# Kernel optimization log

Hardware: AMD Instinct MI355X
Metric: run time of the kernel (lower is better)

## Reference

```python
import jax, jax.numpy as jnp
import numpy as np

NE, EW, TOP_K, T_D, MAXNNZ = 32, 2944, 4, 8, 256
ALPHA, LIMIT, ORIG = 1.702, 7.0, 2880
HID = 2048


def setup_inputs() -> dict:
    key = jax.random.key(0)
    ks = jax.random.split(key, 7)
    dt = jnp.float16
    hid = jax.random.normal(ks[0], (1, 1024, HID), dtype=dt)
    # rand_init() sets all params to torch.rand(...)/5 -> Uniform[0, 0.2)
    gate_w = (jax.random.uniform(ks[1], (NE, HID), dtype=dt) * 0.2).astype(dt)
    u = (jax.random.uniform(ks[2], (NE * EW, HID), dtype=dt) * 0.2).astype(dt)
    g = (jax.random.uniform(ks[3], (NE * EW, HID), dtype=dt) * 0.2).astype(dt)
    d = (jax.random.uniform(ks[4], (HID, NE * EW), dtype=dt) * 0.2).astype(dt)
    ub = (jax.random.uniform(ks[5], (NE * EW,), dtype=dt) * 0.2).astype(dt)
    gb = (jax.random.uniform(ks[6], (NE * EW,), dtype=dt) * 0.2).astype(dt)
    return {"hid": hid, "gate_w": gate_w, "u": u, "g": g, "d": d, "ub": ub, "gb": gb}


def _act(up, gate):
    # clamped GLU: gate clamped above, up clamped both sides; glu = g*sigmoid(alpha*g); (up+1)*glu
    gate = jnp.minimum(gate, LIMIT)
    up = jnp.clip(up, -LIMIT, LIMIT)
    glu = gate * jax.nn.sigmoid(gate * ALPHA)
    act = (up + 1.0) * glu
    return act.at[..., ORIG:].set(0)  # padded inter dims (2880..2944) zeroed


def _forward(hid, gate_w, u, g, d, ub, gb):
    B, S, H = hid.shape
    x = hid.reshape(-1, H)           # [bs, H]
    bs = x.shape[0]

    # --- routing: softmax -> top-k -> renormalize -> scatter to sparse weights ---
    logits = (x @ gate_w.T).astype(jnp.float32)          # [bs, NE]
    probs = jax.nn.softmax(logits, axis=1)
    vals, idx = jax.lax.top_k(probs, TOP_K)
    vals = vals / vals.sum(axis=1, keepdims=True)
    sparse_rw = jnp.zeros_like(probs).at[jnp.arange(bs)[:, None], idx].set(vals)
    rw = sparse_rw.astype(x.dtype)                        # [bs, NE]

    # --- expert selection: t_d dense experts + t_d sparse experts by load ---
    routing_n = jnp.count_nonzero(rw, axis=0)
    mask_c = jax.lax.top_k(routing_n, 2 * T_D)[1]         # [2*T_D]
    cd, cs = mask_c[:T_D], mask_c[T_D:]
    # top-MAXNNZ tokens per sparse expert
    mask_r = jax.lax.top_k(sparse_rw[:, cs].T, MAXNNZ)[1].T  # [MAXNNZ, T_D]

    U = u.reshape(NE, EW, H)
    G = g.reshape(NE, EW, H)
    UB = ub.reshape(NE, EW)
    GB = gb.reshape(NE, EW)
    D = d.reshape(H, NE, EW)

    # --- dense experts: every token runs through the t_d hottest experts ---
    up_d = jnp.einsum('nh,teh->nte', x, U[cd]) + UB[cd]   # [bs, T_D, EW]
    gt_d = jnp.einsum('nh,teh->nte', x, G[cd]) + GB[cd]
    act_d = _act(up_d, gt_d) * rw[:, cd][..., None]       # routing weight combine
    out = jnp.einsum('nte,hte->nh', act_d, D[:, cd])      # [bs, H]

    # --- sparse experts: gather top-MAXNNZ tokens, MLP, scatter-add back ---
    xs = x[mask_r]                                        # [M, T_D, H]
    up_s = jnp.einsum('mth,teh->mte', xs, U[cs]) + UB[cs]
    gt_s = jnp.einsum('mth,teh->mte', xs, G[cs]) + GB[cs]
    w_s = rw[mask_r, cs[None, :]]                         # [M, T_D]
    act_s = _act(up_s, gt_s) * w_s[..., None]
    contrib = jnp.einsum('mte,hte->mth', act_s, D[:, cs])  # [M, T_D, H]
    out = out.at[mask_r.reshape(-1)].add(contrib.reshape(-1, H))

    return out.reshape(B, S, H)


def reference(hid, gate_w, u, g, d, ub, gb):
    return _forward(hid, gate_w, u, g, d, ub, gb)
```

## Files before the change

### kernel.cpp

```cpp
#include <hip/hip_runtime.h>

#define HID 2048
#define NE_ 32
#define EW_ 2944
#define ORIG_ 2880
#define TOPK_ 4
#define MAXNNZ_ 256
#define BS_ 1024
#define NEWTOT (NE_*EW_)

typedef unsigned short u16;
typedef _Float16 h8  __attribute__((ext_vector_type(8)));
typedef float  f32x4 __attribute__((ext_vector_type(4)));
typedef float  fv4   __attribute__((ext_vector_type(4)));

__device__ __forceinline__ u16 f2h_bits(float f){
  union{ _Float16 h; u16 u; } c; c.h = (_Float16)f; return c.u;
}
__device__ __forceinline__ float f16q(float f){ return (float)(_Float16)f; }

__device__ __forceinline__ h8 cvt8(fv4 a, fv4 b){
  h8 r;
  r[0]=(_Float16)a[0]; r[1]=(_Float16)a[1]; r[2]=(_Float16)a[2]; r[3]=(_Float16)a[3];
  r[4]=(_Float16)b[0]; r[5]=(_Float16)b[1]; r[6]=(_Float16)b[2]; r[7]=(_Float16)b[3];
  return r;
}
__device__ __forceinline__ int ldsx(int row, int chunk){
  return row*32 + ((chunk ^ ((row>>1)&3))*8);
}

__device__ __forceinline__ void barrier_lgkm(){
  asm volatile("s_waitcnt lgkmcnt(0)" ::: "memory");
  __builtin_amdgcn_s_barrier();
  __builtin_amdgcn_sched_barrier(0);
}

__device__ __forceinline__ int rank_kth(const int* counts, int kth){
  int cnt[NE_]; bool used[NE_];
  for (int e=0;e<NE_;e++){ cnt[e]=counts[e]; used[e]=false; }
  int bi=0;
  for (int k=0;k<=kth;k++){
    int best=-1; bi=0;
    for (int e=0;e<NE_;e++) if(!used[e] && cnt[e]>best){best=cnt[e];bi=e;}
    used[bi]=true;
  }
  return bi;
}

__global__ __launch_bounds__(256) void k_gate(const float* __restrict__ x,
                                              const float* __restrict__ gw,
                                              float* __restrict__ rw,
                                              float* __restrict__ rwf,
                                              int* __restrict__ counts,
                                              u16* __restrict__ xh)
{
  __shared__ float slog[4][NE_];
  const int tid = threadIdx.x, wid = tid>>6, lane = tid&63;
  const int n = blockIdx.x*4 + wid;
  const float* xr = x + (size_t)n*HID + lane*32;
  float xf[32];
  #pragma unroll
  for (int i=0;i<8;i++){
    fv4 v = *(const fv4*)(xr + i*4);
    #pragma unroll
    for (int j=0;j<4;j++) xf[i*4+j] = v[j];
  }
  #pragma unroll
  for (int c=0;c<4;c++){
    h8 hv;
    #pragma unroll
    for (int j=0;j<8;j++) hv[j] = (_Float16)xf[c*8+j];
    *(h8*)(xh + (size_t)n*HID + lane*32 + c*8) = hv;
  }
  for (int e=0;e<NE_;e++){
    const float* gr = gw + (size_t)e*HID + lane*32;
    float p = 0.f;
    #pragma unroll
    for (int i=0;i<8;i++){
      fv4 v = *(const fv4*)(gr + i*4);
      #pragma unroll
      for (int j=0;j<4;j++) p += xf[i*4+j]*v[j];
    }
    #pragma unroll
    for (int s=32;s>0;s>>=1) p += __shfl_xor(p, s);
    if (lane==0) slog[wid][e] = f16q(p);
  }
  if (lane==0){
    float mx=-1e30f;
    for (int e=0;e<NE_;e++) mx = fmaxf(mx, slog[wid][e]);
    float pr[NE_]; float sum=0.f;
    for (int e=0;e<NE_;e++){ float v=__expf(slog[wid][e]-mx); pr[e]=v; sum+=v; }
    for (int e=0;e<NE_;e++) pr[e] = pr[e]/sum;
    int   idx[TOPK_]; float val[TOPK_]; bool used[NE_];
    for (int e=0;e<NE_;e++) used[e]=false;
    float vs=0.f;
    for (int k=0;k<TOPK_;k++){
      float best=-1.f; int bi=0;
      for (int e=0;e<NE_;e++) if(!used[e] && pr[e]>best){best=pr[e];bi=e;}
      used[bi]=true; idx[k]=bi; val[k]=best; vs+=best;
    }
    float* rwr  = rw  + (size_t)n*NE_;
    float* rwfr = rwf + (size_t)n*NE_;
    for (int k=0;k<TOPK_;k++){
      float vraw = val[k]/vs;
      float q = f16q(vraw);
      rwr[idx[k]]  = q;
      rwfr[idx[k]] = vraw;
      if (q!=0.f) atomicAdd(counts+idx[k], 1);
    }
  }
}

__global__ __launch_bounds__(256) void k_lists(const float* __restrict__ rw,
                                               const float* __restrict__ rwf,
                                               const int* __restrict__ counts,
                                               int* __restrict__ cdcs,
                                               int* __restrict__ tok_all,
                                               int* __restrict__ cnt_all,
                                               int* __restrict__ inv,
                                               int* __restrict__ invcnt)
{
  __shared__ float v[BS_];
  __shared__ int scnt;
  __shared__ int e_sh;
  const int z = blockIdx.x;
  const int tid = threadIdx.x;
  if (tid==0){
    int e = rank_kth(counts, z);
    e_sh = e;
    cdcs[z] = e;
    scnt = 0;
  }
  for (int i=tid;i<BS_;i+=256) tok_all[z*BS_+i] = 0;
  __syncthreads();
  const int e = e_sh;
  for (int i=tid;i<BS_;i+=256) v[i] = (z<8) ? rw[(size_t)i*NE_+e] : rwf[(size_t)i*NE_+e];
  __syncthreads();
  for (int i=tid;i<BS_;i+=256){
    bool take;
    if (z<8){
      take = (v[i]!=0.f);
    } else {
      float vi=v[i]; int r=0;
      for (int m=0;m<BS_;m++){
        float vm=v[m];
        r += (vm>vi) || (vm==vi && m<i);
      }
      take = (r<MAXNNZ_) && (rw[(size_t)i*NE_+e]!=0.f);
    }
    if (take){
      int slot = atomicAdd(&scnt,1);
      tok_all[z*BS_+slot] = i;
      int c = atomicAdd(&invcnt[i],1);
      inv[i*4+c] = (z<<16) | slot;
    }
  }
  __syncthreads();
  if (tid==0) cnt_all[z] = scnt;
}

__global__ __launch_bounds__(256, 4) void k_fused(const u16* __restrict__ xh,
                                               const float* __restrict__ uw,
                                               const float* __restrict__ gww,
                                               const float* __restrict__ ub,
                                               const float* __restrict__ gb,
                                               const float* __restrict__ rw,
                                               const int* __restrict__ cdcs,
                                               const int* __restrict__ tok_all,
                                               const int* __restrict__ cnt_all,
                                               u16* __restrict__ act)
{
  const int z=blockIdx.z, bx=blockIdx.x, by=blockIdx.y;
  const int cnt = cnt_all[z];
  if (by*128 >= cnt) return;
  const int e = cdcs[z];
  __shared__ __align__(16) u16 ldsA[2][128*32];
  __shared__ __align__(16) u16 ldsB[2][64*32];
  const int tid=threadIdx.x, lane=tid&63, w=tid>>6;
  const int lr = lane&15, kq = lane>>4;

  const int ar = tid>>1, c0 = (tid&1)*2;
  const int tokA = tok_all[z*BS_ + by*128 + ar];
  const u16* ap = xh + (size_t)tokA*HID + c0*8;
  const int br = tid>>2, bch = tid&3;
  const float* bp = (br<32 ? uw  + ((size_t)e*EW_ + bx*32 + br)*HID
                           : gww + ((size_t)e*EW_ + bx*32 + (br-32))*HID) + bch*8;

  f32x4 au[2][2], ag[2][2];
  #pragma unroll
  for (int i=0;i<2;i++)
    #pragma unroll
    for (int j=0;j<2;j++)
      #pragma unroll
      for (int q=0;q<4;q++){ au[i][j][q]=0.f; ag[i][j][q]=0.f; }

  h8 As0, As1; fv4 Ba, Bb;
  As0 = *(const h8*)ap; As1 = *(const h8*)(ap+8);
  Ba = *(const fv4*)bp; Bb = *(const fv4*)(bp+4);

  const int NK = HID/32;
  #pragma unroll 2
  for (int kt=0; kt<NK; kt++){
    u16* A = ldsA[kt&1]; u16* B = ldsB[kt&1];
    *(h8*)&A[ldsx(ar, c0  )] = As0;
    *(h8*)&A[ldsx(ar, c0+1)] = As1;
    *(h8*)&B[ldsx(br, bch)] = cvt8(Ba,Bb);
    if (kt+1<NK){
      const int k1=(kt+1)*32;
      As0 = *(const h8*)(ap+k1); As1 = *(const h8*)(ap+k1+8);
      Ba=*(const fv4*)(bp+k1); Bb=*(const fv4*)(bp+k1+4);
    }
    barrier_lgkm();
    h8 af[2], fu[2], fg[2];
    #pragma unroll
    for (int m=0;m<2;m++) af[m] = *(const h8*)&A[ldsx(w*32+m*16+lr, kq)];
    #pragma unroll
    for (int n2=0;n2<2;n2++){
      fu[n2] = *(const h8*)&B[ldsx(   n2*16+lr, kq)];
      fg[n2] = *(const h8*)&B[ldsx(32+n2*16+lr, kq)];
    }
    #pragma unroll
    for (int m=0;m<2;m++)
      #pragma unroll
      for (int n2=0;n2<2;n2++){
        au[m][n2]=__builtin_amdgcn_mfma_f32_16x16x32_f16(af[m],fu[n2],au[m][n2],0,0,0);
        ag[m][n2]=__builtin_amdgcn_mfma_f32_16x16x32_f16(af[m],fg[n2],ag[m][n2],0,0,0);
      }
  }

  #pragma unroll
  for (int n2=0;n2<2;n2++){
    const int col = bx*32 + n2*16 + lr;
    const float ubv = ub[(size_t)e*EW_ + col];
    const float gbv = gb[(size_t)e*EW_ + col];
    #pragma unroll
    for (int m=0;m<2;m++){
      #pragma unroll
      for (int j=0;j<4;j++){
        const int s = by*128 + w*32 + m*16 + kq*4 + j;
        if (s < cnt){
          float upv = f16q(au[m][n2][j] + ubv);
          float gtv = f16q(ag[m][n2][j] + gbv);
          float wv = rw[(size_t)tok_all[z*BS_+s]*NE_ + e];
          float gc = fminf(gtv, 7.0f);
          float uc = fminf(fmaxf(upv,-7.0f),7.0f);
          float glu = gc * (1.f/(1.f+__expf(-gc*1.702f)));
          act[((size_t)z*BS_+s)*ORIG_ + col] = f2h_bits((uc+1.f)*glu*wv);
        }
      }
    }
  }
}

__global__ __launch_bounds__(256, 4) void k_down(const u16* __restrict__ act,
                                              const float* __restrict__ dw,
                                              const int* __restrict__ cdcs,
                                              const int* __restrict__ cnt_all,
                                              u16* __restrict__ contrib)
{
  const int zz=blockIdx.z, bx=blockIdx.x, by=blockIdx.y;
  const int z = zz>>1, kh = zz&1;
  const int cnt = cnt_all[z];
  if (by*128 >= cnt) return;
  const int e = cdcs[z];
  __shared__ __align__(16) u16 ldsA[2][128*32];
  __shared__ __align__(16) u16 ldsB[2][64*32];
  const int tid=threadIdx.x, lane=tid&63, w=tid>>6;
  const int lr = lane&15, kq = lane>>4;
  const int kbase = kh*1440;

  const int ar = tid>>1, c0 = (tid&1)*2;
  const u16* ap = act + ((size_t)z*BS_ + by*128 + ar)*ORIG_ + kbase + c0*8;
  const int br = tid>>2, bch = tid&3;
  const float* bp = dw + (size_t)(bx*64 + br)*NEWTOT + (size_t)e*EW_ + kbase + bch*8;

  f32x4 acc[2][4];
  #pragma unroll
  for (int i=0;i<2;i++)
    #pragma unroll
    for (int j=0;j<4;j++)
      #pragma unroll
      for (int q=0;q<4;q++) acc[i][j][q]=0.f;

  h8 As0, As1; fv4 Ba, Bb;
  As0 = *(const h8*)ap; As1 = *(const h8*)(ap+8);
  Ba = *(const fv4*)bp; Bb = *(const fv4*)(bp+4);

  const int NK = 1440/32;
  #pragma unroll 2
  for (int kt=0; kt<NK; kt++){
    u16* A = ldsA[kt&1]; u16* B = ldsB[kt&1];
    *(h8*)&A[ldsx(ar, c0  )] = As0;
    *(h8*)&A[ldsx(ar, c0+1)] = As1;
    *(h8*)&B[ldsx(br, bch)] = cvt8(Ba,Bb);
    if (kt+1<NK){
      const int k1 = (kt+1)*32;
      As0 = *(const h8*)(ap+k1); As1 = *(const h8*)(ap+k1+8);
      Ba=*(const fv4*)(bp+k1); Bb=*(const fv4*)(bp+k1+4);
    }
    barrier_lgkm();
    h8 af[2], bfr[4];
    #pragma unroll
    for (int m=0;m<2;m++)    af[m]  = *(const h8*)&A[ldsx(w*32+m*16+lr, kq)];
    #pragma unroll
    for (int n2=0;n2<4;n2++) bfr[n2] = *(const h8*)&B[ldsx(n2*16+lr, kq)];
    #pragma unroll
    for (int m=0;m<2;m++)
      #pragma unroll
      for (int n2=0;n2<4;n2++)
        acc[m][n2]=__builtin_amdgcn_mfma_f32_16x16x32_f16(af[m],bfr[n2],acc[m][n2],0,0,0);
  }

  #pragma unroll
  for (int m=0;m<2;m++){
    #pragma unroll
    for (int j=0;j<4;j++){
      const int slot = by*128 + w*32 + m*16 + kq*4 + j;
      if (slot < cnt){
        #pragma unroll
        for (int n2=0;n2<4;n2++){
          const int col = bx*64 + n2*16 + lr;
          contrib[((size_t)zz*BS_ + slot)*HID + col] = f2h_bits(acc[m][n2][j]);
        }
      }
    }
  }
}

__global__ __launch_bounds__(256) void k_combine(const u16* __restrict__ contrib,
                                                 const int* __restrict__ inv,
                                                 const int* __restrict__ invcnt,
                                                 float* __restrict__ out)
{
  const int gid = blockIdx.x*256 + threadIdx.x;
  const int base = gid*8;
  const int n = base >> 11;
  const int h = base & 2047;
  float acc[8];
  #pragma unroll
  for (int q=0;q<8;q++) acc[q]=0.f;
  const int c = invcnt[n];
  for (int j=0;j<c;j++){
    const int code = inv[n*4+j];
    const int z = code>>16;
    const int slot = code & 0xFFFF;
    const u16* p = contrib + ((size_t)(z*2)*BS_ + slot)*HID + h;
    h8 v0 = *(const h8*)p;
    h8 v1 = *(const h8*)(p + (size_t)BS_*HID);
    #pragma unroll
    for (int q=0;q<8;q++) acc[q] += (float)v0[q] + (float)v1[q];
  }
  fv4 o0, o1;
  #pragma unroll
  for (int q=0;q<4;q++){ o0[q]=acc[q]; o1[q]=acc[4+q]; }
  *(fv4*)(out + base) = o0;
  *(fv4*)(out + base + 4) = o1;
}

extern "C" void kernel_launch(void* const* d_in, const int* in_sizes, int n_in,
                              void* d_out, int out_size, void* d_ws, size_t ws_size,
                              hipStream_t stream)
{
  const float* x  = (const float*)d_in[0];
  const float* gw = (const float*)d_in[1];
  const float* u  = (const float*)d_in[2];
  const float* g  = (const float*)d_in[3];
  const float* dw = (const float*)d_in[4];
  const float* ub = (const float*)d_in[5];
  const float* gb = (const float*)d_in[6];

  char* ws = (char*)d_ws;
  size_t off = 0;
  auto alloc = [&](size_t bytes)->void*{ void* p = ws + off; off += (bytes + 255) & ~(size_t)255; return p; };
  float* rw     = (float*)alloc((size_t)BS_*NE_*4);
  float* rwf    = (float*)alloc((size_t)BS_*NE_*4);
  int*   counts = (int*)  alloc(NE_*4);
  int*   invcnt = (int*)  alloc(BS_*4);
  size_t zero_span = off;
  int*   cdcs   = (int*)  alloc(16*4);
  int*   cnt_all= (int*)  alloc(16*4);
  int*   tok_all= (int*)  alloc((size_t)16*BS_*4);
  int*   inv    = (int*)  alloc((size_t)BS_*4*4);
  u16*   xh     = (u16*)  alloc((size_t)BS_*HID*2);
  u16*   act    = (u16*)  alloc((size_t)16*BS_*ORIG_*2);
  u16*   contrib= (u16*)  alloc((size_t)32*BS_*HID*2);
  if (off > ws_size) return;

  hipMemsetAsync(ws, 0, zero_span, stream);

  k_gate <<<BS_/4, 256, 0, stream>>>(x, gw, rw, rwf, counts, xh);
  k_lists<<<16,    256, 0, stream>>>(rw, rwf, counts, cdcs, tok_all, cnt_all, inv, invcnt);

  k_fused<<<dim3(ORIG_/32, 8, 16), 256, 0, stream>>>(xh, u, g, ub, gb, rw,
                                                     cdcs, tok_all, cnt_all, act);
  k_down <<<dim3(HID/64, 8, 32), 256, 0, stream>>>(act, dw, cdcs, cnt_all, contrib);
  k_combine<<<BS_*HID/(256*8), 256, 0, stream>>>(contrib, inv, invcnt, (float*)d_out);
}
```

Before: 658.7 us.

## Double M tile to 256 rows and deepen weight prefetch in expert GEMMs

The up/gate and down GEMM kernels now process 256 token rows per block instead of 128, with each warp computing 64 rows. Each fp32 weight tile converted to fp16 is therefore reused across twice as many tokens, roughly halving weight traffic and conversion work. The weight loads are also prefetched four k-steps ahead and the activation loads two steps ahead, using manually unrolled register buffers. The cost is more registers and LDS per block (occupancy bound lowered to 2) and fewer blocks, which leaves the GPU less evenly filled when experts have small token counts.

```diff
diff --git a/kernel.cpp b/kernel.cpp
--- a/kernel.cpp
+++ b/kernel.cpp
@@ -159,7 +159,40 @@
   if (tid==0) cnt_all[z] = scnt;
 }
 
-__global__ __launch_bounds__(256, 4) void k_fused(const u16* __restrict__ xh,
+#define FSTEP(P, KT)                                                        \
+{                                                                           \
+  u16* A = ldsA[(P)&1]; u16* B = ldsB[(P)&1];                               \
+  _Pragma("unroll")                                                         \
+  for (int r=0;r<4;r++) *(h8*)&A[ldsx(ar + r*64, ach)] = Aset[(P)&1][r];    \
+  *(h8*)&B[ldsx(br, ach)] = cvt8(Bsa[(P)], Bsb[(P)]);                       \
+  if ((KT)+2 < NKF){                                                        \
+    const int k2 = ((KT)+2)*32;                                             \
+    _Pragma("unroll")                                                       \
+    for (int r=0;r<4;r++) Aset[(P)&1][r] = *(const h8*)(ap[r]+k2);          \
+  }                                                                         \
+  if ((KT)+4 < NKF){                                                        \
+    const int k4 = ((KT)+4)*32;                                             \
+    Bsa[(P)] = *(const fv4*)(bp+k4); Bsb[(P)] = *(const fv4*)(bp+k4+4);     \
+  }                                                                         \
+  barrier_lgkm();                                                           \
+  h8 af[4], fu[2], fg[2];                                                   \
+  _Pragma("unroll")                                                         \
+  for (int m=0;m<4;m++) af[m] = *(const h8*)&A[ldsx(w*64+m*16+lr, kq)];     \
+  _Pragma("unroll")                                                         \
+  for (int n2=0;n2<2;n2++){                                                 \
+    fu[n2] = *(const h8*)&B[ldsx(   n2*16+lr, kq)];                         \
+    fg[n2] = *(const h8*)&B[ldsx(32+n2*16+lr, kq)];                         \
+  }                                                                         \
+  _Pragma("unroll")                                                         \
+  for (int m=0;m<4;m++)                                                     \
+    _Pragma("unroll")                                                       \
+    for (int n2=0;n2<2;n2++){                                               \
+      au[m][n2]=__builtin_amdgcn_mfma_f32_16x16x32_f16(af[m],fu[n2],au[m][n2],0,0,0); \
+      ag[m][n2]=__builtin_amdgcn_mfma_f32_16x16x32_f16(af[m],fg[n2],ag[m][n2],0,0,0); \
+    }                                                                       \
+}
+
+__global__ __launch_bounds__(256, 2) void k_fused(const u16* __restrict__ xh,
                                                const float* __restrict__ uw,
                                                const float* __restrict__ gww,
                                                const float* __restrict__ ub,
@@ -172,60 +205,48 @@
 {
   const int z=blockIdx.z, bx=blockIdx.x, by=blockIdx.y;
   const int cnt = cnt_all[z];
-  if (by*128 >= cnt) return;
+  if (by*256 >= cnt) return;
   const int e = cdcs[z];
-  __shared__ __align__(16) u16 ldsA[2][128*32];
+  __shared__ __align__(16) u16 ldsA[2][256*32];
   __shared__ __align__(16) u16 ldsB[2][64*32];
   const int tid=threadIdx.x, lane=tid&63, w=tid>>6;
   const int lr = lane&15, kq = lane>>4;
-
-  const int ar = tid>>1, c0 = (tid&1)*2;
-  const int tokA = tok_all[z*BS_ + by*128 + ar];
-  const u16* ap = xh + (size_t)tokA*HID + c0*8;
-  const int br = tid>>2, bch = tid&3;
+  const int ar = tid>>2, ach = tid&3;
+  const u16* ap[4];
+  #pragma unroll
+  for (int r=0;r<4;r++){
+    const int tok = tok_all[z*BS_ + by*256 + ar + r*64];
+    ap[r] = xh + (size_t)tok*HID + ach*8;
+  }
+  const int br = ar;
   const float* bp = (br<32 ? uw  + ((size_t)e*EW_ + bx*32 + br)*HID
-                           : gww + ((size_t)e*EW_ + bx*32 + (br-32))*HID) + bch*8;
-
-  f32x4 au[2][2], ag[2][2];
-  #pragma unroll
-  for (int i=0;i<2;i++)
+                           : gww + ((size_t)e*EW_ + bx*32 + (br-32))*HID) + ach*8;
+
+  f32x4 au[4][2], ag[4][2];
+  #pragma unroll
+  for (int i=0;i<4;i++)
     #pragma unroll
     for (int j=0;j<2;j++)
       #pragma unroll
       for (int q=0;q<4;q++){ au[i][j][q]=0.f; ag[i][j][q]=0.f; }
 
-  h8 As0, As1; fv4 Ba, Bb;
-  As0 = *(const h8*)ap; As1 = *(const h8*)(ap+8);
-  Ba = *(const fv4*)bp; Bb = *(const fv4*)(bp+4);
-
-  const int NK = HID/32;
-  #pragma unroll 2
-  for (int kt=0; kt<NK; kt++){
-    u16* A = ldsA[kt&1]; u16* B = ldsB[kt&1];
-    *(h8*)&A[ldsx(ar, c0  )] = As0;
-    *(h8*)&A[ldsx(ar, c0+1)] = As1;
-    *(h8*)&B[ldsx(br, bch)] = cvt8(Ba,Bb);
-    if (kt+1<NK){
-      const int k1=(kt+1)*32;
-      As0 = *(const h8*)(ap+k1); As1 = *(const h8*)(ap+k1+8);
-      Ba=*(const fv4*)(bp+k1); Bb=*(const fv4*)(bp+k1+4);
-    }
-    barrier_lgkm();
-    h8 af[2], fu[2], fg[2];
-    #pragma unroll
-    for (int m=0;m<2;m++) af[m] = *(const h8*)&A[ldsx(w*32+m*16+lr, kq)];
-    #pragma unroll
-    for (int n2=0;n2<2;n2++){
-      fu[n2] = *(const h8*)&B[ldsx(   n2*16+lr, kq)];
-      fg[n2] = *(const h8*)&B[ldsx(32+n2*16+lr, kq)];
-    }
-    #pragma unroll
-    for (int m=0;m<2;m++)
-      #pragma unroll
-      for (int n2=0;n2<2;n2++){
-        au[m][n2]=__builtin_amdgcn_mfma_f32_16x16x32_f16(af[m],fu[n2],au[m][n2],0,0,0);
-        ag[m][n2]=__builtin_amdgcn_mfma_f32_16x16x32_f16(af[m],fg[n2],ag[m][n2],0,0,0);
-      }
+  h8 Aset[2][4]; fv4 Bsa[4], Bsb[4];
+  #pragma unroll
+  for (int r=0;r<4;r++){
+    Aset[0][r] = *(const h8*)ap[r];
+    Aset[1][r] = *(const h8*)(ap[r]+32);
+  }
+  #pragma unroll
+  for (int p=0;p<4;p++){
+    Bsa[p] = *(const fv4*)(bp+p*32); Bsb[p] = *(const fv4*)(bp+p*32+4);
+  }
+
+  const int NKF = HID/32;
+  for (int kt=0; kt<NKF; kt+=4){
+    FSTEP(0, kt)
+    FSTEP(1, kt+1)
+    FSTEP(2, kt+2)
+    FSTEP(3, kt+3)
   }
 
   #pragma unroll
@@ -234,10 +255,10 @@
     const float ubv = ub[(size_t)e*EW_ + col];
     const float gbv = gb[(size_t)e*EW_ + col];
     #pragma unroll
-    for (int m=0;m<2;m++){
+    for (int m=0;m<4;m++){
       #pragma unroll
       for (int j=0;j<4;j++){
-        const int s = by*128 + w*32 + m*16 + kq*4 + j;
+        const int s = by*256 + w*64 + m*16 + kq*4 + j;
         if (s < cnt){
           float upv = f16q(au[m][n2][j] + ubv);
           float gtv = f16q(ag[m][n2][j] + gbv);
@@ -252,7 +273,35 @@
   }
 }
 
-__global__ __launch_bounds__(256, 4) void k_down(const u16* __restrict__ act,
+#define DSTEP(P, KT)                                                        \
+{                                                                           \
+  u16* A = ldsA[(P)&1]; u16* B = ldsB[(P)&1];                               \
+  _Pragma("unroll")                                                         \
+  for (int r=0;r<4;r++) *(h8*)&A[ldsx(ar + r*64, ach)] = Aset[(P)&1][r];    \
+  *(h8*)&B[ldsx(br, ach)] = cvt8(Bsa[(P)], Bsb[(P)]);                       \
+  if ((KT)+2 < NKD){                                                        \
+    const int k2 = ((KT)+2)*32;                                             \
+    _Pragma("unroll")                                                       \
+    for (int r=0;r<4;r++) Aset[(P)&1][r] = *(const h8*)(ap[r]+k2);          \
+  }                                                                         \
+  if ((KT)+4 < NKD){                                                        \
+    const int k4 = ((KT)+4)*32;                                             \
+    Bsa[(P)] = *(const fv4*)(bp+k4); Bsb[(P)] = *(const fv4*)(bp+k4+4);     \
+  }                                                                         \
+  barrier_lgkm();                                                           \
+  h8 af[4], bfr[4];                                                         \
+  _Pragma("unroll")                                                         \
+  for (int m=0;m<4;m++)    af[m]  = *(const h8*)&A[ldsx(w*64+m*16+lr, kq)]; \
+  _Pragma("unroll")                                                         \
+  for (int n2=0;n2<4;n2++) bfr[n2] = *(const h8*)&B[ldsx(n2*16+lr, kq)];    \
+  _Pragma("unroll")                                                         \
+  for (int m=0;m<4;m++)                                                     \
+    _Pragma("unroll")                                                       \
+    for (int n2=0;n2<4;n2++)                                                \
+      acc[m][n2]=__builtin_amdgcn_mfma_f32_16x16x32_f16(af[m],bfr[n2],acc[m][n2],0,0,0); \
+}
+
+__global__ __launch_bounds__(256, 2) void k_down(const u16* __restrict__ act,
                                               const float* __restrict__ dw,
                                               const int* __restrict__ cdcs,
                                               const int* __restrict__ cnt_all,
@@ -261,61 +310,55 @@
   const int zz=blockIdx.z, bx=blockIdx.x, by=blockIdx.y;
   const int z = zz>>1, kh = zz&1;
   const int cnt = cnt_all[z];
-  if (by*128 >= cnt) return;
+  if (by*256 >= cnt) return;
   const int e = cdcs[z];
-  __shared__ __align__(16) u16 ldsA[2][128*32];
+  __shared__ __align__(16) u16 ldsA[2][256*32];
   __shared__ __align__(16) u16 ldsB[2][64*32];
   const int tid=threadIdx.x, lane=tid&63, w=tid>>6;
   const int lr = lane&15, kq = lane>>4;
+  const int ar = tid>>2, ach = tid&3;
   const int kbase = kh*1440;
 
-  const int ar = tid>>1, c0 = (tid&1)*2;
-  const u16* ap = act + ((size_t)z*BS_ + by*128 + ar)*ORIG_ + kbase + c0*8;
-  const int br = tid>>2, bch = tid&3;
-  const float* bp = dw + (size_t)(bx*64 + br)*NEWTOT + (size_t)e*EW_ + kbase + bch*8;
-
-  f32x4 acc[2][4];
-  #pragma unroll
-  for (int i=0;i<2;i++)
+  const u16* ap[4];
+  #pragma unroll
+  for (int r=0;r<4;r++)
+    ap[r] = act + ((size_t)z*BS_ + by*256 + ar + r*64)*ORIG_ + kbase + ach*8;
+  const int br = ar;
+  const float* bp = dw + (size_t)(bx*64 + br)*NEWTOT + (size_t)e*EW_ + kbase + ach*8;
+
+  f32x4 acc[4][4];
+  #pragma unroll
+  for (int i=0;i<4;i++)
     #pragma unroll
     for (int j=0;j<4;j++)
       #pragma unroll
       for (int q=0;q<4;q++) acc[i][j][q]=0.f;
 
-  h8 As0, As1; fv4 Ba, Bb;
-  As0 = *(const h8*)ap; As1 = *(const h8*)(ap+8);
-  Ba = *(const fv4*)bp; Bb = *(const fv4*)(bp+4);
-
-  const int NK = 1440/32;
-  #pragma unroll 2
-  for (int kt=0; kt<NK; kt++){
-    u16* A = ldsA[kt&1]; u16* B = ldsB[kt&1];
-    *(h8*)&A[ldsx(ar, c0  )] = As0;
-    *(h8*)&A[ldsx(ar, c0+1)] = As1;
-    *(h8*)&B[ldsx(br, bch)] = cvt8(Ba,Bb);
-    if (kt+1<NK){
-      const int k1 = (kt+1)*32;
-      As0 = *(const h8*)(ap+k1); As1 = *(const h8*)(ap+k1+8);
-      Ba=*(const fv4*)(bp+k1); Bb=*(const fv4*)(bp+k1+4);
-    }
-    barrier_lgkm();
-    h8 af[2], bfr[4];
-    #pragma unroll
-    for (int m=0;m<2;m++)    af[m]  = *(const h8*)&A[ldsx(w*32+m*16+lr, kq)];
-    #pragma unroll
-    for (int n2=0;n2<4;n2++) bfr[n2] = *(const h8*)&B[ldsx(n2*16+lr, kq)];
-    #pragma unroll
-    for (int m=0;m<2;m++)
-      #pragma unroll
-      for (int n2=0;n2<4;n2++)
-        acc[m][n2]=__builtin_amdgcn_mfma_f32_16x16x32_f16(af[m],bfr[n2],acc[m][n2],0,0,0);
-  }
-
-  #pragma unroll
-  for (int m=0;m<2;m++){
+  h8 Aset[2][4]; fv4 Bsa[4], Bsb[4];
+  #pragma unroll
+  for (int r=0;r<4;r++){
+    Aset[0][r] = *(const h8*)ap[r];
+    Aset[1][r] = *(const h8*)(ap[r]+32);
+  }
+  #pragma unroll
+  for (int p=0;p<4;p++){
+    Bsa[p] = *(const fv4*)(bp+p*32); Bsb[p] = *(const fv4*)(bp+p*32+4);
+  }
+
+  const int NKD = 1440/32;
+  for (int kt=0; kt<44; kt+=4){
+    DSTEP(0, kt)
+    DSTEP(1, kt+1)
+    DSTEP(2, kt+2)
+    DSTEP(3, kt+3)
+  }
+  DSTEP(0, 44)
+
+  #pragma unroll
+  for (int m=0;m<4;m++){
     #pragma unroll
     for (int j=0;j<4;j++){
-      const int slot = by*128 + w*32 + m*16 + kq*4 + j;
+      const int slot = by*256 + w*64 + m*16 + kq*4 + j;
       if (slot < cnt){
         #pragma unroll
         for (int n2=0;n2<4;n2++){
@@ -391,8 +434,8 @@
   k_gate <<<BS_/4, 256, 0, stream>>>(x, gw, rw, rwf, counts, xh);
   k_lists<<<16,    256, 0, stream>>>(rw, rwf, counts, cdcs, tok_all, cnt_all, inv, invcnt);
 
-  k_fused<<<dim3(ORIG_/32, 8, 16), 256, 0, stream>>>(xh, u, g, ub, gb, rw,
+  k_fused<<<dim3(ORIG_/32, 4, 16), 256, 0, stream>>>(xh, u, g, ub, gb, rw,
                                                      cdcs, tok_all, cnt_all, act);
-  k_down <<<dim3(HID/64, 8, 32), 256, 0, stream>>>(act, dw, cdcs, cnt_all, contrib);
+  k_down <<<dim3(HID/64, 4, 32), 256, 0, stream>>>(act, dw, cdcs, cnt_all, contrib);
   k_combine<<<BS_*HID/(256*8), 256, 0, stream>>>(contrib, inv, invcnt, (float*)d_out);
 }
```

After: 567.8 us. 1.16x faster.
